# Optimization experiments

Measured on AMD Instinct MI355X. Metric: run time of the kernel, lower is better.

## Reference

```python
import jax, jax.numpy as jnp
import numpy as np

DIM = 1024
HEADS = 8


def setup_inputs() -> dict:
    key = jax.random.key(0)
    ks = jax.random.split(key, 8)
    b, n, m, nc, d = 2, 1024, 4, 1024, DIM
    x = jax.random.normal(ks[0], (b, n, d), dtype=jnp.float32)
    context = jax.random.normal(ks[1], (b, m, nc, d), dtype=jnp.float32)
    doc_similarities = jax.random.normal(ks[2], (b, m), dtype=jnp.float32)
    # learned params (Linear weights stored as [in, out] for x @ W)
    s = 1.0 / np.sqrt(d)
    Wq = jax.random.uniform(ks[3], (d, d), minval=-s, maxval=s, dtype=jnp.float32)
    Wkv = jax.random.uniform(ks[4], (d, 2 * d), minval=-s, maxval=s, dtype=jnp.float32)
    Wout = jax.random.uniform(ks[5], (d, d), minval=-s, maxval=s, dtype=jnp.float32)
    bout = jax.random.uniform(ks[6], (d,), minval=-s, maxval=s, dtype=jnp.float32)
    beta = jnp.array(1.0, dtype=jnp.float32)
    return {"x": x, "context": context, "doc_similarities": doc_similarities,
            "Wq": Wq, "Wkv": Wkv, "beta": beta, "Wout": Wout, "bout": bout}


def reference(x, context, doc_similarities, Wq, Wkv, beta, Wout, bout):
    b, n, dim = x.shape
    h = HEADS
    hd = dim // h
    scale = dim ** -0.5
    m, nc = context.shape[1], context.shape[2]

    # q: [b, h, n, hd]
    q = (x @ Wq).reshape(b, n, h, hd).transpose(0, 2, 1, 3)

    # flatten docs: [b, m*nc, dim]
    ctx = context.reshape(b, m * nc, dim)
    # doc similarity bias, repeated per token within each doc: [b, m*nc]
    sim = jnp.repeat(doc_similarities, nc, axis=1) * beta

    kv = ctx @ Wkv  # [b, L, 2*dim]
    k, v = jnp.split(kv, 2, axis=-1)
    k = k.reshape(b, m * nc, h, hd).transpose(0, 2, 1, 3)  # [b, h, L, hd]
    v = v.reshape(b, m * nc, h, hd).transpose(0, 2, 1, 3)

    dots = jnp.einsum('bhid,bhjd->bhij', q, k) * scale
    dots = dots + sim[:, None, None, :]
    attn = jax.nn.softmax(dots, axis=-1)
    out = jnp.einsum('bhij,bhjd->bhid', attn, v)
    out = out.transpose(0, 2, 1, 3).reshape(b, n, dim)
    return out @ Wout + bout
```

## Files before the change

### kernel.cpp

```cpp
#include <hip/hip_runtime.h>
#include <stdint.h>

typedef __attribute__((ext_vector_type(4))) float f32x4;
typedef __attribute__((ext_vector_type(8))) __bf16 bf16x8;

__device__ __forceinline__ uint16_t f2bf(float f) {
  uint32_t u = __builtin_bit_cast(uint32_t, f);
  u += 0x7FFFu + ((u >> 16) & 1u);
  return (uint16_t)(u >> 16);
}

__device__ __forceinline__ float bf2f(uint16_t u) {
  uint32_t v = ((uint32_t)u) << 16;
  return __builtin_bit_cast(float, v);
}

__device__ __forceinline__ void load_lds16(const uint16_t* g, uint16_t* l) {
  __builtin_amdgcn_global_load_lds((const __attribute__((address_space(1))) void*)g,
                                   (__attribute__((address_space(3))) void*)l, 16, 0, 0);
}

__global__ __launch_bounds__(256) void k_prep(const float* __restrict__ x,
                                              const float* __restrict__ ctx,
                                              const float* __restrict__ Wq,
                                              const float* __restrict__ Wkv,
                                              const float* __restrict__ Wout,
                                              uint16_t* __restrict__ xb,
                                              uint16_t* __restrict__ ctxb,
                                              uint16_t* __restrict__ wqt,
                                              uint16_t* __restrict__ wkvt,
                                              uint16_t* __restrict__ woutt,
                                              float qscale) {
  __shared__ float tile[32][33];
  int id = blockIdx.x;
  int tid = threadIdx.x;
  if (id < 10240) {
    const float* in;
    uint16_t* out;
    int j = id * 256 + tid;
    if (j < 524288) { in = x; out = xb; }
    else            { in = ctx; out = ctxb; j -= 524288; }
    float4 v = ((const float4*)in)[j];
    union { uint16_t u[4]; uint64_t q; } o;
    o.u[0] = f2bf(v.x); o.u[1] = f2bf(v.y); o.u[2] = f2bf(v.z); o.u[3] = f2bf(v.w);
    ((uint64_t*)out)[j] = o.q;
    return;
  }
  id -= 10240;
  const float* W;
  uint16_t* Wt;
  int N, n0, k0;
  float sc = 1.0f;
  if (id < 1024)      { W = Wq;   Wt = wqt;   N = 1024; sc = qscale;
                        n0 = (id & 31) * 32; k0 = (id >> 5) * 32; }
  else if (id < 2048) { W = Wout; Wt = woutt; N = 1024; id -= 1024;
                        n0 = (id & 31) * 32; k0 = (id >> 5) * 32; }
  else                { W = Wkv;  Wt = wkvt;  N = 2048; id -= 2048;
                        n0 = (id & 63) * 32; k0 = (id >> 6) * 32; }
  int c = tid & 31, r0 = tid >> 5;
#pragma unroll
  for (int i = 0; i < 4; i++) {
    int r = r0 + i * 8;
    tile[r][c] = W[(size_t)(k0 + r) * N + n0 + c];
  }
  __syncthreads();
#pragma unroll
  for (int i = 0; i < 4; i++) {
    int r = r0 + i * 8;
    Wt[(size_t)(n0 + r) * 1024 + k0 + c] = f2bf(tile[c][r] * sc);
  }
}

__global__ __launch_bounds__(256) void k_gemm_fused(const uint16_t* __restrict__ ctxb,
                                                    const uint16_t* __restrict__ wkvt,
                                                    const uint16_t* __restrict__ xb,
                                                    const uint16_t* __restrict__ wqt,
                                                    uint16_t* __restrict__ kb,
                                                    uint16_t* __restrict__ vtb,
                                                    uint16_t* __restrict__ qb) {
  __shared__ uint16_t smem[9216];
  uint16_t* la = smem;
  uint16_t* lb = smem + 4096;
  const int K = 1024;
  const int tid = threadIdx.x;
  const int lane = tid & 63, w = tid >> 6;
  const int quad = lane >> 4, l16 = lane & 15;
  const int wr = (w >> 1) * 64, wc = (w & 1) * 64;
  int id = blockIdx.x;
  int bx, by, isQ;
  const uint16_t *Ab, *Bb;
  if (id < 1024) {
    isQ = 0;
    int xcd = id & 7, t = id >> 3;
    by = (xcd << 3) + (t & 7);
    bx = t >> 3;
    Ab = ctxb + (size_t)by * 128 * K;
    Bb = wkvt + (size_t)bx * 128 * K;
  } else {
    isQ = 1; id -= 1024;
    int xcd = id & 7, t = id >> 3;
    by = (xcd << 1) + (t & 1);
    bx = t >> 1;
    Ab = xb + (size_t)by * 128 * K;
    Bb = wqt + (size_t)bx * 128 * K;
  }
  f32x4 acc[4][4] = {};
  const int rA = tid >> 2, slotA = tid & 3;
  const int rA1 = rA + 64;
  const int segA0 = (slotA ^ ((rA + (rA >> 2)) & 3)) * 8;
  const int segA1 = (slotA ^ ((rA1 + (rA1 >> 2)) & 3)) * 8;
  for (int k0 = 0; k0 < K; k0 += 32) {
    __syncthreads();
    load_lds16(Ab + (size_t)rA * K + k0 + segA0, la + tid * 8);
    load_lds16(Ab + (size_t)rA1 * K + k0 + segA1, la + (tid + 256) * 8);
    load_lds16(Bb + (size_t)rA * K + k0 + segA0, lb + tid * 8);
    load_lds16(Bb + (size_t)rA1 * K + k0 + segA1, lb + (tid + 256) * 8);
    __syncthreads();
    bf16x8 af[4], bfr[4];
#pragma unroll
    for (int i = 0; i < 4; i++) {
      int R = wr + i * 16 + l16;
      int s = quad ^ ((R + (R >> 2)) & 3);
      af[i] = *(const bf16x8*)&la[R * 32 + s * 8];
    }
#pragma unroll
    for (int j = 0; j < 4; j++) {
      int R = wc + j * 16 + l16;
      int s = quad ^ ((R + (R >> 2)) & 3);
      bfr[j] = *(const bf16x8*)&lb[R * 32 + s * 8];
    }
#pragma unroll
    for (int i = 0; i < 4; i++)
#pragma unroll
      for (int j = 0; j < 4; j++)
        acc[i][j] = __builtin_amdgcn_mfma_f32_16x16x32_bf16(af[i], bfr[j], acc[i][j], 0, 0, 0);
  }
  __syncthreads();
  if (isQ) {
#pragma unroll
    for (int i = 0; i < 4; i++)
#pragma unroll
      for (int j = 0; j < 4; j++) {
        size_t row = (size_t)by * 128 + wr + i * 16 + quad * 4;
        size_t col = (size_t)bx * 128 + wc + j * 16 + l16;
#pragma unroll
        for (int r = 0; r < 4; r++)
          qb[(row + r) * 1024 + col] = f2bf(acc[i][j][r]);
      }
  } else if (bx < 8) {
#pragma unroll
    for (int i = 0; i < 4; i++)
#pragma unroll
      for (int j = 0; j < 4; j++) {
        int rowg = by * 128 + wr + i * 16 + quad * 4;
        int bb = rowg >> 12, l = rowg & 4095;
        int c = wc + j * 16 + l16;
        uint16_t* dst = kb + (((size_t)(bb * 8 + bx) * 4096 + l) * 128 + c);
#pragma unroll
        for (int r = 0; r < 4; r++)
          dst[r * 128] = f2bf(acc[i][j][r]);
      }
  } else {
    const int bh = (by >> 5) * 8 + (bx - 8);
    const int lbase = (by & 31) * 128;
    uint16_t* vdst = vtb + (size_t)bh * 524288;
#pragma unroll
    for (int half = 0; half < 2; half++) {
      if (wr == half * 64) {
#pragma unroll
        for (int i = 0; i < 4; i++)
#pragma unroll
          for (int j = 0; j < 4; j++) {
            int rowl = i * 16 + quad * 4;
            int col = wc + j * 16 + l16;
            union { uint64_t q; uint16_t u[4]; } pk;
#pragma unroll
            for (int r = 0; r < 4; r++) pk.u[r] = f2bf(acc[i][j][r]);
            *(uint64_t*)&smem[col * 72 + rowl] = pk.q;
          }
      }
      __syncthreads();
      {
        int col = tid >> 1, rseg = (tid & 1) * 32;
        const uint16_t* src = &smem[col * 72 + rseg];
        uint16_t* d = vdst + (size_t)col * 4096 + lbase + half * 64 + rseg;
#pragma unroll
        for (int k = 0; k < 4; k++)
          ((uint4*)d)[k] = *(const uint4*)&src[k * 8];
      }
      __syncthreads();
    }
  }
}

__global__ __launch_bounds__(256) void k_gemm64(const uint16_t* __restrict__ A,
                                                const uint16_t* __restrict__ Bt,
                                                float* __restrict__ Cf,
                                                const float* __restrict__ bias,
                                                int M, int N, int K) {
  __shared__ uint16_t la[64 * 64];
  __shared__ uint16_t lb[64 * 64];
  const int tid = threadIdx.x;
  const int lane = tid & 63, w = tid >> 6;
  const int quad = lane >> 4, l16 = lane & 15;
  const int wr = (w >> 1) * 32, wc = (w & 1) * 32;
  const size_t tr0 = (size_t)blockIdx.y * 64, tc0 = (size_t)blockIdx.x * 64;
  f32x4 acc[2][2] = {};
  const int rS = tid >> 3, sS = tid & 7;
  const int seg = (sS ^ (rS & 7)) * 8;
  const uint16_t* Ab = A + tr0 * K;
  const uint16_t* Bb = Bt + tc0 * K;
  for (int k0 = 0; k0 < K; k0 += 64) {
    __syncthreads();
    load_lds16(Ab + (size_t)rS * K + k0 + seg, la + tid * 8);
    load_lds16(Ab + (size_t)(rS + 32) * K + k0 + seg, la + (tid + 256) * 8);
    load_lds16(Bb + (size_t)rS * K + k0 + seg, lb + tid * 8);
    load_lds16(Bb + (size_t)(rS + 32) * K + k0 + seg, lb + (tid + 256) * 8);
    __syncthreads();
#pragma unroll
    for (int sub = 0; sub < 2; sub++) {
      const int kk = sub * 4 + quad;
      bf16x8 af[2], bfr[2];
#pragma unroll
      for (int i = 0; i < 2; i++) {
        int R = wr + i * 16 + l16;
        af[i] = *(const bf16x8*)&la[R * 64 + (kk ^ (R & 7)) * 8];
      }
#pragma unroll
      for (int j = 0; j < 2; j++) {
        int R = wc + j * 16 + l16;
        bfr[j] = *(const bf16x8*)&lb[R * 64 + (kk ^ (R & 7)) * 8];
      }
#pragma unroll
      for (int i = 0; i < 2; i++)
#pragma unroll
        for (int j = 0; j < 2; j++)
          acc[i][j] = __builtin_amdgcn_mfma_f32_16x16x32_bf16(af[i], bfr[j], acc[i][j], 0, 0, 0);
    }
  }
#pragma unroll
  for (int i = 0; i < 2; i++) {
#pragma unroll
    for (int j = 0; j < 2; j++) {
      size_t row = tr0 + wr + i * 16 + quad * 4;
      size_t col = tc0 + wc + j * 16 + l16;
#pragma unroll
      for (int r = 0; r < 4; r++)
        Cf[(row + r) * N + col] = acc[i][j][r] + bias[col];
    }
  }
}

__global__ __launch_bounds__(256) void k_attn(const uint16_t* __restrict__ q,
                                              const uint16_t* __restrict__ kb,
                                              const uint16_t* __restrict__ vt,
                                              const float* __restrict__ sims,
                                              const float* __restrict__ beta,
                                              uint16_t* __restrict__ po,
                                              float* __restrict__ pl) {
  __shared__ uint16_t Kl[8192];
  __shared__ uint16_t Vl[8192];
  __shared__ uint16_t Pl[4096];
  const int idx = blockIdx.x;
  const int qbx = idx >> 7, g = idx & 127;
  const int h = g >> 4, b = (g >> 3) & 1, sp = g & 7;
  const int q0 = qbx * 128;
  const int tid = threadIdx.x, lane = tid & 63, w = tid >> 6;
  const int quad = lane >> 4, l16 = lane & 15;
  const float wsplit =
      __builtin_amdgcn_exp2f(sims[b * 4 + (sp >> 1)] * beta[0] * 1.44269504f);
  uint16_t* Pw = Pl + w * 1024;

  union { uint32_t u[4]; bf16x8 v; } Oc;
#pragma unroll
  for (int j = 0; j < 4; j++) Oc.u[j] = 0x3F803F80u;
  const bf16x8 onesf = Oc.v;

  bf16x8 qf[2][4];
#pragma unroll
  for (int rb = 0; rb < 2; rb++) {
    const uint16_t* qrow =
        q + ((size_t)(b * 1024 + q0 + w * 32 + rb * 16 + l16)) * 1024 + h * 128 + quad * 8;
#pragma unroll
    for (int ks = 0; ks < 4; ks++) qf[rb][ks] = *(const bf16x8*)(qrow + ks * 32);
  }
  f32x4 o[2][8] = {};
  f32x4 o9[2] = {};

  const uint16_t* kptr = kb + ((size_t)(b * 8 + h) * 4096 + sp * 512) * 128;
  const uint16_t* vptr = vt + ((size_t)(b * 8 + h) * 128) * 4096 + sp * 512;

  for (int c = 0; c < 8; c++) {
    __syncthreads();
#pragma unroll
    for (int ii = 0; ii < 4; ii++) {
      int g2 = tid + ii * 256;
      int row = g2 >> 4, seg = (g2 & 15) ^ (row & 15);
      load_lds16(kptr + row * 128 + seg * 8, Kl + g2 * 8);
    }
#pragma unroll
    for (int ii = 0; ii < 4; ii++) {
      int g2 = tid + ii * 256;
      int row = g2 >> 3, seg = (g2 & 7) ^ (row & 7);
      load_lds16(vptr + (size_t)row * 4096 + seg * 8, Vl + g2 * 8);
    }
    __syncthreads();
#pragma unroll
    for (int kh = 0; kh < 2; kh++) {
#pragma unroll
      for (int nb2 = 0; nb2 < 2; nb2++) {
        const int nb = kh * 2 + nb2;
        f32x4 s0 = {}, s1 = {};
#pragma unroll
        for (int ks = 0; ks < 4; ks++) {
          bf16x8 kf = *(const bf16x8*)&Kl[(nb * 16 + l16) * 128 + (((ks * 4 + quad) ^ l16) * 8)];
          s0 = __builtin_amdgcn_mfma_f32_16x16x32_bf16(qf[0][ks], kf, s0, 0, 0, 0);
          s1 = __builtin_amdgcn_mfma_f32_16x16x32_bf16(qf[1][ks], kf, s1, 0, 0, 0);
        }
        const int sl = nb2 * 2 + (l16 >> 3);
#pragma unroll
        for (int r = 0; r < 4; r++) {
          int rp0 = quad * 4 + r;
          Pw[rp0 * 32 + ((sl ^ ((rp0 >> 1) & 3)) * 8) + (l16 & 7)] =
              f2bf(__builtin_amdgcn_exp2f(s0[r]));
          int rp1 = 16 + rp0;
          Pw[rp1 * 32 + ((sl ^ ((rp1 >> 1) & 3)) * 8) + (l16 & 7)] =
              f2bf(__builtin_amdgcn_exp2f(s1[r]));
        }
      }
      __asm__ volatile("s_waitcnt lgkmcnt(0)" ::: "memory");
      const int segp = (quad ^ ((l16 >> 1) & 3)) * 8;
      bf16x8 pf0 = *(const bf16x8*)&Pw[l16 * 32 + segp];
      bf16x8 pf1 = *(const bf16x8*)&Pw[(16 + l16) * 32 + segp];
      const int sq = ((kh * 4 + quad) ^ (l16 & 7)) * 8;
#pragma unroll
      for (int nb = 0; nb < 8; nb++) {
        bf16x8 vf = *(const bf16x8*)&Vl[(nb * 16 + l16) * 64 + sq];
        o[0][nb] = __builtin_amdgcn_mfma_f32_16x16x32_bf16(pf0, vf, o[0][nb], 0, 0, 0);
        o[1][nb] = __builtin_amdgcn_mfma_f32_16x16x32_bf16(pf1, vf, o[1][nb], 0, 0, 0);
      }
      o9[0] = __builtin_amdgcn_mfma_f32_16x16x32_bf16(pf0, onesf, o9[0], 0, 0, 0);
      o9[1] = __builtin_amdgcn_mfma_f32_16x16x32_bf16(pf1, onesf, o9[1], 0, 0, 0);
    }
    kptr += 64 * 128;
    vptr += 64;
  }
  const int rowbase = (sp * 16 + b * 8 + h) * 1024 + q0 + w * 32;
#pragma unroll
  for (int rb = 0; rb < 2; rb++)
#pragma unroll
    for (int r = 0; r < 4; r++) {
      int row = rowbase + rb * 16 + quad * 4 + r;
#pragma unroll
      for (int nb = 0; nb < 8; nb++)
        po[(size_t)row * 128 + nb * 16 + l16] = f2bf(o[rb][nb][r] * wsplit);
      if (l16 == 0)
        pl[row] = o9[rb][r] * wsplit;
    }
}

__global__ __launch_bounds__(256) void k_merge(const uint16_t* __restrict__ po,
                                               const float* __restrict__ pl,
                                               uint16_t* __restrict__ attb) {
  const int bq = blockIdx.x;
  const int b = bq >> 10, qi = bq & 1023;
  const int t = threadIdx.x;
  const int h = t >> 5, d0 = (t & 31) * 4;
  const int bh = b * 8 + h;
  float den = 0.f;
  float acc[4] = {0.f, 0.f, 0.f, 0.f};
#pragma unroll
  for (int s = 0; s < 8; s++) {
    den += pl[(s * 16 + bh) * 1024 + qi];
    union { uint64_t q; uint16_t u[4]; } v;
    v.q = *(const uint64_t*)&po[(((size_t)(s * 16 + bh)) * 1024 + qi) * 128 + d0];
#pragma unroll
    for (int j = 0; j < 4; j++) acc[j] += bf2f(v.u[j]);
  }
  const float inv = 1.0f / den;
  union { uint64_t q; uint16_t u[4]; } o;
#pragma unroll
  for (int j = 0; j < 4; j++) o.u[j] = f2bf(acc[j] * inv);
  *(uint64_t*)&attb[((size_t)(b * 1024 + qi)) * 1024 + h * 128 + d0] = o.q;
}

extern "C" void kernel_launch(void* const* d_in, const int* in_sizes, int n_in,
                              void* d_out, int out_size, void* d_ws, size_t ws_size,
                              hipStream_t stream) {
  (void)in_sizes; (void)n_in; (void)out_size; (void)ws_size;
  const float* x    = (const float*)d_in[0];
  const float* ctx  = (const float*)d_in[1];
  const float* sims = (const float*)d_in[2];
  const float* Wq   = (const float*)d_in[3];
  const float* Wkv  = (const float*)d_in[4];
  const float* beta = (const float*)d_in[5];
  const float* Wout = (const float*)d_in[6];
  const float* bout = (const float*)d_in[7];
  float* out = (float*)d_out;

  char* ws = (char*)d_ws;
  uint16_t* xb    = (uint16_t*)(ws + 0);
  uint16_t* ctxb  = (uint16_t*)(ws + (4u << 20));
  uint16_t* wqt   = (uint16_t*)(ws + (20u << 20));
  uint16_t* wkvt  = (uint16_t*)(ws + (22u << 20));
  uint16_t* kb    = (uint16_t*)(ws + (32u << 20));
  uint16_t* vtb   = (uint16_t*)(ws + (48u << 20));
  float*    pl    = (float*)   (ws + (64u << 20));
  uint16_t* woutt = (uint16_t*)(ws + (68u << 20));
  uint16_t* qb    = (uint16_t*)(ws + (70u << 20));
  uint16_t* attb  = (uint16_t*)(ws + (74u << 20));
  uint16_t* po = (uint16_t*)(ws + 0);

  const float LOG2E = 1.44269504f;
  const float qscale = 0.03125f * LOG2E;

  k_prep<<<14336, 256, 0, stream>>>(x, ctx, Wq, Wkv, Wout, xb, ctxb, wqt, wkvt, woutt, qscale);
  k_gemm_fused<<<1152, 256, 0, stream>>>(ctxb, wkvt, xb, wqt, kb, vtb, qb);
  k_attn<<<1024, 256, 0, stream>>>(qb, kb, vtb, sims, beta, po, pl);
  k_merge<<<2048, 256, 0, stream>>>(po, pl, attb);
  k_gemm64<<<dim3(16, 32), 256, 0, stream>>>(attb, woutt, out, bout, 2048, 1024, 1024);
}
```

Baseline: 232.1 us.

## Double-buffer LDS tiles in GEMM kernels to overlap global loads with MFMA

Both projection GEMM kernels switch from a single LDS buffer, filled and synchronized each k-step, to a ping-pong double buffer. The next tile is prefetched with global_load_lds while the current one is consumed, using explicit vmcnt waits and barriers. It also raises wave priority around the MFMA block and adds an occupancy hint to the fused GEMM. The aim is to hide global-memory latency in the K loop, at the cost of twice the LDS per block, which may reduce occupancy.

```diff
diff --git a/kernel.cpp b/kernel.cpp
--- a/kernel.cpp
+++ b/kernel.cpp
@@ -71,16 +71,14 @@
   }
 }
 
-__global__ __launch_bounds__(256) void k_gemm_fused(const uint16_t* __restrict__ ctxb,
-                                                    const uint16_t* __restrict__ wkvt,
-                                                    const uint16_t* __restrict__ xb,
-                                                    const uint16_t* __restrict__ wqt,
-                                                    uint16_t* __restrict__ kb,
-                                                    uint16_t* __restrict__ vtb,
-                                                    uint16_t* __restrict__ qb) {
-  __shared__ uint16_t smem[9216];
-  uint16_t* la = smem;
-  uint16_t* lb = smem + 4096;
+__global__ __launch_bounds__(256, 4) void k_gemm_fused(const uint16_t* __restrict__ ctxb,
+                                                       const uint16_t* __restrict__ wkvt,
+                                                       const uint16_t* __restrict__ xb,
+                                                       const uint16_t* __restrict__ wqt,
+                                                       uint16_t* __restrict__ kb,
+                                                       uint16_t* __restrict__ vtb,
+                                                       uint16_t* __restrict__ qb) {
+  __shared__ uint16_t smem[16384];
   const int K = 1024;
   const int tid = threadIdx.x;
   const int lane = tid & 63, w = tid >> 6;
@@ -109,13 +107,28 @@
   const int rA1 = rA + 64;
   const int segA0 = (slotA ^ ((rA + (rA >> 2)) & 3)) * 8;
   const int segA1 = (slotA ^ ((rA1 + (rA1 >> 2)) & 3)) * 8;
-  for (int k0 = 0; k0 < K; k0 += 32) {
-    __syncthreads();
-    load_lds16(Ab + (size_t)rA * K + k0 + segA0, la + tid * 8);
-    load_lds16(Ab + (size_t)rA1 * K + k0 + segA1, la + (tid + 256) * 8);
-    load_lds16(Bb + (size_t)rA * K + k0 + segA0, lb + tid * 8);
-    load_lds16(Bb + (size_t)rA1 * K + k0 + segA1, lb + (tid + 256) * 8);
-    __syncthreads();
+  const uint16_t* gA0 = Ab + (size_t)rA * K + segA0;
+  const uint16_t* gA1 = Ab + (size_t)rA1 * K + segA1;
+  const uint16_t* gB0 = Bb + (size_t)rA * K + segA0;
+  const uint16_t* gB1 = Bb + (size_t)rA1 * K + segA1;
+  load_lds16(gA0, smem + tid * 8);
+  load_lds16(gA1, smem + (tid + 256) * 8);
+  load_lds16(gB0, smem + (tid + 512) * 8);
+  load_lds16(gB1, smem + (tid + 768) * 8);
+  for (int t = 0; t < 32; ++t) {
+    const uint16_t* la = smem + (t & 1) * 8192;
+    const uint16_t* lb = la + 4096;
+    if (t < 31) {
+      uint16_t* ln = smem + ((t + 1) & 1) * 8192;
+      const int k1 = (t + 1) * 32;
+      load_lds16(gA0 + k1, ln + tid * 8);
+      load_lds16(gA1 + k1, ln + (tid + 256) * 8);
+      load_lds16(gB0 + k1, ln + (tid + 512) * 8);
+      load_lds16(gB1 + k1, ln + (tid + 768) * 8);
+      asm volatile("s_waitcnt vmcnt(4)\n\ts_barrier" ::: "memory");
+    } else {
+      asm volatile("s_waitcnt vmcnt(0)\n\ts_barrier" ::: "memory");
+    }
     bf16x8 af[4], bfr[4];
 #pragma unroll
     for (int i = 0; i < 4; i++) {
@@ -129,11 +142,14 @@
       int s = quad ^ ((R + (R >> 2)) & 3);
       bfr[j] = *(const bf16x8*)&lb[R * 32 + s * 8];
     }
+    __builtin_amdgcn_s_setprio(1);
 #pragma unroll
     for (int i = 0; i < 4; i++)
 #pragma unroll
       for (int j = 0; j < 4; j++)
         acc[i][j] = __builtin_amdgcn_mfma_f32_16x16x32_bf16(af[i], bfr[j], acc[i][j], 0, 0, 0);
+    __builtin_amdgcn_s_setprio(0);
+    asm volatile("s_barrier" ::: "memory");
   }
   __syncthreads();
   if (isQ) {
@@ -198,8 +214,7 @@
                                                 float* __restrict__ Cf,
                                                 const float* __restrict__ bias,
                                                 int M, int N, int K) {
-  __shared__ uint16_t la[64 * 64];
-  __shared__ uint16_t lb[64 * 64];
+  __shared__ uint16_t smem[16384];
   const int tid = threadIdx.x;
   const int lane = tid & 63, w = tid >> 6;
   const int quad = lane >> 4, l16 = lane & 15;
@@ -210,13 +225,30 @@
   const int seg = (sS ^ (rS & 7)) * 8;
   const uint16_t* Ab = A + tr0 * K;
   const uint16_t* Bb = Bt + tc0 * K;
-  for (int k0 = 0; k0 < K; k0 += 64) {
-    __syncthreads();
-    load_lds16(Ab + (size_t)rS * K + k0 + seg, la + tid * 8);
-    load_lds16(Ab + (size_t)(rS + 32) * K + k0 + seg, la + (tid + 256) * 8);
-    load_lds16(Bb + (size_t)rS * K + k0 + seg, lb + tid * 8);
-    load_lds16(Bb + (size_t)(rS + 32) * K + k0 + seg, lb + (tid + 256) * 8);
-    __syncthreads();
+  const uint16_t* gA0 = Ab + (size_t)rS * K + seg;
+  const uint16_t* gA1 = Ab + (size_t)(rS + 32) * K + seg;
+  const uint16_t* gB0 = Bb + (size_t)rS * K + seg;
+  const uint16_t* gB1 = Bb + (size_t)(rS + 32) * K + seg;
+  const int NT = K >> 6;
+  load_lds16(gA0, smem + tid * 8);
+  load_lds16(gA1, smem + (tid + 256) * 8);
+  load_lds16(gB0, smem + (tid + 512) * 8);
+  load_lds16(gB1, smem + (tid + 768) * 8);
+  for (int t = 0; t < NT; ++t) {
+    const uint16_t* la = smem + (t & 1) * 8192;
+    const uint16_t* lb = la + 4096;
+    if (t < NT - 1) {
+      uint16_t* ln = smem + ((t + 1) & 1) * 8192;
+      const int k1 = (t + 1) * 64;
+      load_lds16(gA0 + k1, ln + tid * 8);
+      load_lds16(gA1 + k1, ln + (tid + 256) * 8);
+      load_lds16(gB0 + k1, ln + (tid + 512) * 8);
+      load_lds16(gB1 + k1, ln + (tid + 768) * 8);
+      asm volatile("s_waitcnt vmcnt(4)\n\ts_barrier" ::: "memory");
+    } else {
+      asm volatile("s_waitcnt vmcnt(0)\n\ts_barrier" ::: "memory");
+    }
+    __builtin_amdgcn_s_setprio(1);
 #pragma unroll
     for (int sub = 0; sub < 2; sub++) {
       const int kk = sub * 4 + quad;
@@ -237,6 +269,8 @@
         for (int j = 0; j < 2; j++)
           acc[i][j] = __builtin_amdgcn_mfma_f32_16x16x32_bf16(af[i], bfr[j], acc[i][j], 0, 0, 0);
     }
+    __builtin_amdgcn_s_setprio(0);
+    asm volatile("s_barrier" ::: "memory");
   }
 #pragma unroll
   for (int i = 0; i < 2; i++) {
```

After: 221.8 us. -4.4%, faster.
